# Performance work log

Hardware: AMD Instinct MI355X
Metric: run time of the kernel (lower is better)

## Reference

```python
import jax, jax.numpy as jnp
import numpy as np

NB_OBJ = 3
DIM_BODY = 10
DIM_OBJ = 15
DIM_LEMB = 100
PHI_IN = DIM_LEMB + DIM_BODY + 2 * (NB_OBJ + DIM_OBJ)  # 146
HID = 256
PHI_OUT = 256
ACT_DIM = 4
BATCH = 65536
LOG_SIG_MIN, LOG_SIG_MAX = -20.0, 2.0
# permutations of 3 objects taken 2: (0,1),(0,2),(1,0),(1,2),(2,0),(2,1)
IDX_I = np.array([0, 0, 1, 1, 2, 2])
IDX_J = np.array([1, 2, 0, 2, 0, 1])


def _xavier(key, fan_in, fan_out):
    lim = float(np.sqrt(6.0 / (fan_in + fan_out)))
    return jax.random.uniform(key, (fan_in, fan_out), jnp.float32, -lim, lim)


def setup_inputs() -> dict:
    key = jax.random.key(0)
    ks = jax.random.split(key, 8)
    return {
        "obs": jax.random.normal(ks[0], (BATCH, DIM_BODY + NB_OBJ * DIM_OBJ), jnp.float32),
        "l_emb": jax.random.normal(ks[1], (BATCH, DIM_LEMB), jnp.float32),
        "phi_w1": _xavier(ks[2], PHI_IN, HID), "phi_b1": jnp.zeros((HID,), jnp.float32),
        "phi_w2": _xavier(ks[3], HID, PHI_OUT), "phi_b2": jnp.zeros((PHI_OUT,), jnp.float32),
        "rho_w1": _xavier(ks[4], PHI_OUT, HID), "rho_b1": jnp.zeros((HID,), jnp.float32),
        "mean_w": _xavier(ks[5], HID, ACT_DIM), "mean_b": jnp.zeros((ACT_DIM,), jnp.float32),
        "lstd_w": _xavier(ks[6], HID, ACT_DIM), "lstd_b": jnp.zeros((ACT_DIM,), jnp.float32),
    }


def reference(obs, l_emb, phi_w1, phi_b1, phi_w2, phi_b2,
              rho_w1, rho_b1, mean_w, mean_b, lstd_w, lstd_b):
    B = obs.shape[0]
    obs_body = obs[:, :DIM_BODY]                                   # [B, 10]
    obj_feats = obs[:, DIM_BODY:].reshape(B, NB_OBJ, DIM_OBJ)      # [B, 3, 15]
    one_hot = jnp.broadcast_to(jnp.eye(NB_OBJ, dtype=obs.dtype)[None], (B, NB_OBJ, NB_OBJ))
    objs = jnp.concatenate([one_hot, obj_feats], axis=-1)          # [B, 3, 18]
    base = jnp.concatenate([l_emb, obs_body], axis=-1)             # [B, 110]
    # pairwise concat over the 6 ordered pairs -> [6, B, 146]
    xi = objs[:, IDX_I].transpose(1, 0, 2)                         # [6, B, 18]
    xj = objs[:, IDX_J].transpose(1, 0, 2)
    base6 = jnp.broadcast_to(base[None], (6, B, base.shape[-1]))
    inp = jnp.concatenate([base6, xi, xj], axis=-1)                # [6, B, 146]
    # phi MLP
    h = jax.nn.relu(jnp.einsum('pbi,ih->pbh', inp, phi_w1) + phi_b1)
    h = jax.nn.relu(jnp.einsum('pbh,ho->pbo', h, phi_w2) + phi_b2)
    agg = h.sum(axis=0)                                            # [B, 256]
    # rho MLP
    r = jax.nn.relu(agg @ rho_w1 + rho_b1)
    mean = r @ mean_w + mean_b
    log_std = jnp.clip(r @ lstd_w + lstd_b, LOG_SIG_MIN, LOG_SIG_MAX)
    return mean, log_std
```

## Files before the change

kernel.cpp:

```cpp
#include <hip/hip_runtime.h>

#define BATCH 65536
#define TB 32

typedef _Float16 half8 __attribute__((ext_vector_type(8)));
typedef _Float16 half4v __attribute__((ext_vector_type(4)));
typedef _Float16 half2v __attribute__((ext_vector_type(2)));
typedef float fx4 __attribute__((ext_vector_type(4)));

#define PW1B_OFF 0
#define PW1F_OFF 32768
#define PW2_OFF  40960
#define PWR_OFF  106496
#define PWH_OFF  172032
#define WS_TOTAL 176128

__global__ __launch_bounds__(256) void prep_weights(
    const float* __restrict__ w1, const float* __restrict__ w2,
    const float* __restrict__ wr, const float* __restrict__ wm,
    const float* __restrict__ wl, _Float16* __restrict__ ws)
{
  int idx = blockIdx.x * 256 + threadIdx.x;
  if (idx < 32768) {
    int kk = idx & 31, n = (idx >> 5) & 255, kt = idx >> 13;
    int k = kt * 32 + kk;
    ws[idx] = (k < 110) ? (_Float16)w1[k * 256 + n] : (_Float16)0.f;
  } else if (idx < 40960) {
    int t = idx - 32768;
    int kk = t & 31, n = t >> 5;
    _Float16 v = (_Float16)0.f;
    if (kk < 15)                  v = (_Float16)w1[(113 + kk) * 256 + n];
    else if (kk >= 16 && kk < 31) v = (_Float16)w1[(131 + (kk - 16)) * 256 + n];
    ws[idx] = v;
  } else if (idx < 106496) {
    int t = idx - 40960;
    int kk = t & 31, n = (t >> 5) & 255, kt = t >> 13;
    ws[idx] = (_Float16)w2[(kt * 32 + kk) * 256 + n];
  } else if (idx < 172032) {
    int t = idx - 106496;
    int kk = t & 31, n = (t >> 5) & 255, kt = t >> 13;
    ws[idx] = (_Float16)wr[(kt * 32 + kk) * 256 + n];
  } else if (idx < WS_TOTAL) {
    int t = idx - 172032;
    int kk = t & 31, n = (t >> 5) & 15, kt = t >> 9;
    int k = kt * 32 + kk;
    _Float16 v = (_Float16)0.f;
    if (n < 4) v = (_Float16)wm[k * 4 + n];
    else if (n < 8) v = (_Float16)wl[k * 4 + (n - 4)];
    ws[PWH_OFF + t] = v;
  }
}

__global__ __launch_bounds__(512) void actor_fused(
    const float* __restrict__ obs, const float* __restrict__ lemb,
    const float* __restrict__ w1, const _Float16* __restrict__ ws,
    const float* __restrict__ b1, const float* __restrict__ b2,
    const float* __restrict__ br, const float* __restrict__ bm,
    const float* __restrict__ bl, float* __restrict__ out)
{
  __shared__ __align__(16) _Float16 H1[6 * 16 * 256];
  __shared__ __align__(16) _Float16 Bb[32 * 256];
  __shared__ __align__(16) _Float16 Os[3 * 32 * 16];
  __shared__ __align__(16) float    Bsf[6 * 256];

  const _Float16* __restrict__ pw1b = ws + PW1B_OFF;
  const _Float16* __restrict__ pw1f = ws + PW1F_OFF;
  const _Float16* __restrict__ pw2  = ws + PW2_OFF;
  const _Float16* __restrict__ pwr  = ws + PWR_OFF;
  const _Float16* __restrict__ pwh  = ws + PWH_OFF;

  const int tid  = threadIdx.x;
  const int wave = tid >> 6;
  const int lane = tid & 63;
  const int q    = lane >> 4;
  const int l16  = lane & 15;
  const int colbase = wave * 32;
  const int rowbase = blockIdx.x * TB;

  const int c0_0 = colbase + q * 4;
  const int c0_1 = colbase + 16 + q * 4;

  for (int idx = tid; idx < 1024; idx += 512) {
    int oct = idx >> 6;
    int r   = (idx >> 1) & 31;
    int hf  = idx & 1;
    int c   = oct * 8 + hf * 4;
    float v0, v1, v2, v3;
    if (c + 3 < 100) {
      float4 f = *(const float4*)(lemb + (rowbase + r) * 100 + c);
      v0 = f.x; v1 = f.y; v2 = f.z; v3 = f.w;
    } else {
      const float* orow = obs + (rowbase + r) * 55;
      const float* lrow = lemb + (rowbase + r) * 100;
      float t[4];
      #pragma unroll
      for (int j = 0; j < 4; ++j) {
        int cc = c + j;
        t[j] = cc < 100 ? lrow[cc] : (cc < 110 ? orow[cc - 100] : 0.f);
      }
      v0 = t[0]; v1 = t[1]; v2 = t[2]; v3 = t[3];
    }
    half4v hv = {(_Float16)v0, (_Float16)v1, (_Float16)v2, (_Float16)v3};
    *(half4v*)&Bb[(oct * 32 + r) * 8 + hf * 4] = hv;
  }
  for (int idx = tid; idx < 384; idx += 512) {
    int o   = idx >> 7;
    int k4i = (idx >> 5) & 3;
    int r   = idx & 31;
    int k0  = k4i * 4;
    const float* frow = obs + (rowbase + r) * 55 + 10 + o * 15;
    float t[4];
    #pragma unroll
    for (int j = 0; j < 4; ++j) {
      int k = k0 + j;
      t[j] = (k < 15) ? frow[k] : 0.f;
    }
    half4v hv = {(_Float16)t[0], (_Float16)t[1], (_Float16)t[2], (_Float16)t[3]};
    *(half4v*)&Os[o * 512 + ((k0 >> 3) * 32 + r) * 8 + (k0 & 7)] = hv;
  }
  for (int idx = tid; idx < 1536; idx += 512) {
    int p = idx >> 8, c = idx & 255;
    int oi = p >> 1, oj = (1161 >> (2 * p)) & 3;
    Bsf[idx] = b1[c] + w1[(110 + oi) * 256 + c] + w1[(128 + oj) * 256 + c];
  }
  __syncthreads();

  const fx4 zero4 = {0.f, 0.f, 0.f, 0.f};

  fx4 u[4];
  u[0] = zero4; u[1] = zero4; u[2] = zero4; u[3] = zero4;
  #pragma unroll
  for (int kt = 0; kt < 4; ++kt) {
    half8 a0 = *(const half8*)&Bb[((kt * 4 + q) * 32 + l16) * 8];
    half8 a1 = *(const half8*)&Bb[((kt * 4 + q) * 32 + 16 + l16) * 8];
    #pragma unroll
    for (int nt = 0; nt < 2; ++nt) {
      half8 b = *(const half8*)&pw1b[(kt * 256 + colbase + nt * 16 + l16) * 32 + q * 8];
      u[nt]     = __builtin_amdgcn_mfma_f32_16x16x32_f16(b, a0, u[nt], 0, 0, 0);
      u[2 + nt] = __builtin_amdgcn_mfma_f32_16x16x32_f16(b, a1, u[2 + nt], 0, 0, 0);
    }
  }

  auto g1_group = [&](int g) {
    half8 b1f0 = *(const half8*)&pw1f[(colbase + l16) * 32 + q * 8];
    half8 b1f1 = *(const half8*)&pw1f[(colbase + 16 + l16) * 32 + q * 8];
    #pragma unroll
    for (int pp = 0; pp < 3; ++pp) {
      const int p = g * 3 + pp;
      const int oi = p >> 1, oj = (1161 >> (2 * p)) & 3;
      const int o = (q < 2) ? oi : oj;
      #pragma unroll
      for (int rt = 0; rt < 2; ++rt) {
        half8 af = *(const half8*)&Os[o * 512 + ((q & 1) * 32 + rt * 16 + l16) * 8];
        #pragma unroll
        for (int nt = 0; nt < 2; ++nt) {
          fx4 t = __builtin_amdgcn_mfma_f32_16x16x32_f16(nt ? b1f1 : b1f0, af,
                                                         u[rt * 2 + nt], 0, 0, 0);
          const int c0 = nt ? c0_1 : c0_0;
          fx4 bs = *(const fx4*)&Bsf[p * 256 + c0];
          half4v hv = {(_Float16)fmaxf(t[0] + bs[0], 0.f),
                       (_Float16)fmaxf(t[1] + bs[1], 0.f),
                       (_Float16)fmaxf(t[2] + bs[2], 0.f),
                       (_Float16)fmaxf(t[3] + bs[3], 0.f)};
          *(half4v*)&H1[(pp * 2 + rt) * 4096 + ((c0 >> 3) * 16 + l16) * 8 + (c0 & 7)] = hv;
        }
      }
    }
  };

  fx4 agg[4];
  agg[0] = zero4; agg[1] = zero4; agg[2] = zero4; agg[3] = zero4;

  auto g2_group = [&]() {
    #pragma unroll
    for (int nt = 0; nt < 2; ++nt) {
      const int c0 = nt ? c0_1 : c0_0;
      fx4 bv = *(const fx4*)&b2[c0];
      fx4 acc[6];
      #pragma unroll
      for (int i = 0; i < 6; ++i) acc[i] = bv;
      #pragma unroll 2
      for (int kt = 0; kt < 8; ++kt) {
        half8 bb = *(const half8*)&pw2[(kt * 256 + colbase + nt * 16 + l16) * 32 + q * 8];
        #pragma unroll
        for (int t6 = 0; t6 < 6; ++t6) {
          half8 a = *(const half8*)&H1[t6 * 4096 + ((kt * 4 + q) * 16 + l16) * 8];
          acc[t6] = __builtin_amdgcn_mfma_f32_16x16x32_f16(bb, a, acc[t6], 0, 0, 0);
        }
      }
      #pragma unroll
      for (int t6 = 0; t6 < 6; ++t6)
        #pragma unroll
        for (int rr = 0; rr < 4; ++rr)
          agg[(t6 & 1) * 2 + nt][rr] += fmaxf(acc[t6][rr], 0.f);
    }
  };

  g1_group(0);
  __syncthreads();
  g2_group();
  __syncthreads();
  g1_group(1);
  __syncthreads();
  g2_group();

  #pragma unroll
  for (int rt = 0; rt < 2; ++rt)
    #pragma unroll
    for (int nt = 0; nt < 2; ++nt) {
      const int c0 = nt ? c0_1 : c0_0;
      fx4 t = agg[rt * 2 + nt];
      half4v hv = {(_Float16)t[0], (_Float16)t[1], (_Float16)t[2], (_Float16)t[3]};
      *(half4v*)&Bb[((c0 >> 3) * 32 + rt * 16 + l16) * 8 + (c0 & 7)] = hv;
    }
  __syncthreads();

  fx4 acc3[4];
  {
    fx4 brv0 = *(const fx4*)&br[c0_0];
    fx4 brv1 = *(const fx4*)&br[c0_1];
    acc3[0] = brv0; acc3[1] = brv1; acc3[2] = brv0; acc3[3] = brv1;
  }
  #pragma unroll 2
  for (int kt = 0; kt < 8; ++kt) {
    half8 a0 = *(const half8*)&Bb[((kt * 4 + q) * 32 + l16) * 8];
    half8 a1 = *(const half8*)&Bb[((kt * 4 + q) * 32 + 16 + l16) * 8];
    half8 b0 = *(const half8*)&pwr[(kt * 256 + colbase + l16) * 32 + q * 8];
    half8 b1h = *(const half8*)&pwr[(kt * 256 + colbase + 16 + l16) * 32 + q * 8];
    acc3[0] = __builtin_amdgcn_mfma_f32_16x16x32_f16(b0,  a0, acc3[0], 0, 0, 0);
    acc3[1] = __builtin_amdgcn_mfma_f32_16x16x32_f16(b1h, a0, acc3[1], 0, 0, 0);
    acc3[2] = __builtin_amdgcn_mfma_f32_16x16x32_f16(b0,  a1, acc3[2], 0, 0, 0);
    acc3[3] = __builtin_amdgcn_mfma_f32_16x16x32_f16(b1h, a1, acc3[3], 0, 0, 0);
  }
  #pragma unroll
  for (int rt = 0; rt < 2; ++rt)
    #pragma unroll
    for (int nt = 0; nt < 2; ++nt) {
      const int c0 = nt ? c0_1 : c0_0;
      fx4 t = acc3[rt * 2 + nt];
      half4v hv = {(_Float16)fmaxf(t[0], 0.f), (_Float16)fmaxf(t[1], 0.f),
                   (_Float16)fmaxf(t[2], 0.f), (_Float16)fmaxf(t[3], 0.f)};
      *(half4v*)&H1[rt * 4096 + ((c0 >> 3) * 16 + l16) * 8 + (c0 & 7)] = hv;
    }
  __syncthreads();

  if (wave < 2) {
    fx4 a4 = zero4;
    #pragma unroll 2
    for (int kt = 0; kt < 8; ++kt) {
      half8 rfrag = *(const half8*)&H1[wave * 4096 + ((kt * 4 + q) * 16 + l16) * 8];
      half8 wfrag = *(const half8*)&pwh[(kt * 16 + l16) * 32 + q * 8];
      a4 = __builtin_amdgcn_mfma_f32_16x16x32_f16(wfrag, rfrag, a4, 0, 0, 0);
    }
    const int row = rowbase + wave * 16 + l16;
    if (q == 0) {
      fx4 bm4 = *(const fx4*)bm;
      fx4 o = {a4[0] + bm4[0], a4[1] + bm4[1], a4[2] + bm4[2], a4[3] + bm4[3]};
      *(fx4*)&out[row * 4] = o;
    } else if (q == 1) {
      fx4 bl4 = *(const fx4*)bl;
      fx4 o;
      #pragma unroll
      for (int rr = 0; rr < 4; ++rr) {
        float v = a4[rr] + bl4[rr];
        o[rr] = v < -20.f ? -20.f : (v > 2.f ? 2.f : v);
      }
      *(fx4*)&out[BATCH * 4 + row * 4] = o;
    }
  }
}

extern "C" void kernel_launch(void* const* d_in, const int* in_sizes, int n_in,
                              void* d_out, int out_size, void* d_ws, size_t ws_size,
                              hipStream_t stream) {
  const float* obs  = (const float*)d_in[0];
  const float* lemb = (const float*)d_in[1];
  const float* w1   = (const float*)d_in[2];
  const float* b1   = (const float*)d_in[3];
  const float* w2   = (const float*)d_in[4];
  const float* b2   = (const float*)d_in[5];
  const float* wr   = (const float*)d_in[6];
  const float* br   = (const float*)d_in[7];
  const float* wm   = (const float*)d_in[8];
  const float* bm   = (const float*)d_in[9];
  const float* wl   = (const float*)d_in[10];
  const float* bl   = (const float*)d_in[11];
  float* out = (float*)d_out;
  _Float16* ws = (_Float16*)d_ws;

  hipLaunchKernelGGL(prep_weights, dim3(WS_TOTAL / 256), dim3(256), 0, stream,
                     w1, w2, wr, wm, wl, ws);
  hipLaunchKernelGGL(actor_fused, dim3(BATCH / TB), dim3(512), 0, stream,
                     obs, lemb, w1, (const _Float16*)ws, b1, b2, br, bm, bl, out);
}
```

Measured before the change: 215.9 us.

## Switch phi layer-2 GEMM to 32x32x16 MFMA with half-precision aggregation

Replaces the 16x16x32 MFMA tiling of the second phi layer with 32x32x16 MFMA instructions. Each wave now covers 32 output columns by 32 rows per pass and runs the pairs in two chunks (two accumulators, then one) to limit register pressure. The running pair-sum is kept in fp16 registers instead of fp32, which saves registers but adds rounding error across the six summed pairs. The aim is fewer LDS fragment loads per MFMA and better register usage. Weight fragments are reloaded from global memory for the second chunk.

Measured after the change: 195.6 us. -9.4%, faster.

```diff
diff --git a/kernel.cpp b/kernel.cpp
--- a/kernel.cpp
+++ b/kernel.cpp
@@ -7,6 +7,7 @@
 typedef _Float16 half4v __attribute__((ext_vector_type(4)));
 typedef _Float16 half2v __attribute__((ext_vector_type(2)));
 typedef float fx4 __attribute__((ext_vector_type(4)));
+typedef float fx16 __attribute__((ext_vector_type(16)));
 
 #define PW1B_OFF 0
 #define PW1F_OFF 32768
@@ -74,7 +75,10 @@
   const int lane = tid & 63;
   const int q    = lane >> 4;
   const int l16  = lane & 15;
+  const int m31  = lane & 31;
+  const int koct = lane >> 5;
   const int colbase = wave * 32;
+  const int cb8  = colbase >> 3;
   const int rowbase = blockIdx.x * TB;
 
   const int c0_0 = colbase + q * 4;
@@ -168,51 +172,82 @@
     }
   };
 
-  fx4 agg[4];
-  agg[0] = zero4; agg[1] = zero4; agg[2] = zero4; agg[3] = zero4;
-
-  auto g2_group = [&]() {
-    #pragma unroll
-    for (int nt = 0; nt < 2; ++nt) {
-      const int c0 = nt ? c0_1 : c0_0;
-      fx4 bv = *(const fx4*)&b2[c0];
-      fx4 acc[6];
-      #pragma unroll
-      for (int i = 0; i < 6; ++i) acc[i] = bv;
-      #pragma unroll 2
-      for (int kt = 0; kt < 8; ++kt) {
-        half8 bb = *(const half8*)&pw2[(kt * 256 + colbase + nt * 16 + l16) * 32 + q * 8];
+  half4v aggp[4];
+  {
+    half4v z = {(_Float16)0.f, (_Float16)0.f, (_Float16)0.f, (_Float16)0.f};
+    aggp[0] = z; aggp[1] = z; aggp[2] = z; aggp[3] = z;
+  }
+
+  const int brt = m31 >> 4;
+  const int r16 = m31 & 15;
+  auto g2_group = [&](int g) {
+    (void)g;
+    fx16 acc0, acc1;
+    #pragma unroll
+    for (int i = 0; i < 16; ++i) { acc0[i] = 0.f; acc1[i] = 0.f; }
+    #pragma unroll
+    for (int kt = 0; kt < 16; ++kt) {
+      half8 aW = *(const half8*)&pw2[((kt >> 1) * 256 + colbase + m31) * 32 + (kt & 1) * 16 + koct * 8];
+      half8 x0 = *(const half8*)&H1[(0 * 2 + brt) * 4096 + ((kt * 2 + koct) * 16 + r16) * 8];
+      half8 x1 = *(const half8*)&H1[(1 * 2 + brt) * 4096 + ((kt * 2 + koct) * 16 + r16) * 8];
+      acc0 = __builtin_amdgcn_mfma_f32_32x32x16_f16(aW, x0, acc0, 0, 0, 0);
+      acc1 = __builtin_amdgcn_mfma_f32_32x32x16_f16(aW, x1, acc1, 0, 0, 0);
+    }
+    {
+      fx4 bvq[4];
+      #pragma unroll
+      for (int rq = 0; rq < 4; ++rq) bvq[rq] = *(const fx4*)&b2[colbase + rq * 8 + koct * 4];
+      #pragma unroll
+      for (int rq = 0; rq < 4; ++rq) {
+        half4v hp = aggp[rq];
         #pragma unroll
-        for (int t6 = 0; t6 < 6; ++t6) {
-          half8 a = *(const half8*)&H1[t6 * 4096 + ((kt * 4 + q) * 16 + l16) * 8];
-          acc[t6] = __builtin_amdgcn_mfma_f32_16x16x32_f16(bb, a, acc[t6], 0, 0, 0);
+        for (int j = 0; j < 4; ++j) {
+          int i = rq * 4 + j;
+          float b = bvq[rq][j];
+          float s = (float)hp[j] + fmaxf(acc0[i] + b, 0.f) + fmaxf(acc1[i] + b, 0.f);
+          hp[j] = (_Float16)s;
         }
-      }
-      #pragma unroll
-      for (int t6 = 0; t6 < 6; ++t6)
+        aggp[rq] = hp;
+      }
+    }
+    fx16 acc2;
+    #pragma unroll
+    for (int i = 0; i < 16; ++i) acc2[i] = 0.f;
+    #pragma unroll
+    for (int kt = 0; kt < 16; ++kt) {
+      half8 aW = *(const half8*)&pw2[((kt >> 1) * 256 + colbase + m31) * 32 + (kt & 1) * 16 + koct * 8];
+      half8 x2 = *(const half8*)&H1[(2 * 2 + brt) * 4096 + ((kt * 2 + koct) * 16 + r16) * 8];
+      acc2 = __builtin_amdgcn_mfma_f32_32x32x16_f16(aW, x2, acc2, 0, 0, 0);
+    }
+    {
+      fx4 bvq[4];
+      #pragma unroll
+      for (int rq = 0; rq < 4; ++rq) bvq[rq] = *(const fx4*)&b2[colbase + rq * 8 + koct * 4];
+      #pragma unroll
+      for (int rq = 0; rq < 4; ++rq) {
+        half4v hp = aggp[rq];
         #pragma unroll
-        for (int rr = 0; rr < 4; ++rr)
-          agg[(t6 & 1) * 2 + nt][rr] += fmaxf(acc[t6][rr], 0.f);
+        for (int j = 0; j < 4; ++j) {
+          int i = rq * 4 + j;
+          float s = (float)hp[j] + fmaxf(acc2[i] + bvq[rq][j], 0.f);
+          hp[j] = (_Float16)s;
+        }
+        aggp[rq] = hp;
+      }
     }
   };
 
   g1_group(0);
   __syncthreads();
-  g2_group();
+  g2_group(0);
   __syncthreads();
   g1_group(1);
   __syncthreads();
-  g2_group();
+  g2_group(1);
 
   #pragma unroll
-  for (int rt = 0; rt < 2; ++rt)
-    #pragma unroll
-    for (int nt = 0; nt < 2; ++nt) {
-      const int c0 = nt ? c0_1 : c0_0;
-      fx4 t = agg[rt * 2 + nt];
-      half4v hv = {(_Float16)t[0], (_Float16)t[1], (_Float16)t[2], (_Float16)t[3]};
-      *(half4v*)&Bb[((c0 >> 3) * 32 + rt * 16 + l16) * 8 + (c0 & 7)] = hv;
-    }
+  for (int rq = 0; rq < 4; ++rq)
+    *(half4v*)&Bb[((cb8 + rq) * 32 + m31) * 8 + koct * 4] = aggp[rq];
   __syncthreads();
 
   fx4 acc3[4];
```
